# Kernel optimization log

Hardware: AMD Instinct MI355X
Metric: run time of the kernel (lower is better)

## Reference

```python
import jax, jax.numpy as jnp
import numpy as np

B, S, D, H = 2, 2048, 1024, 16
HD = D // H
EPS = 1e-5


def setup_inputs() -> dict:
    key = jax.random.key(0)
    ks = jax.random.split(key, 12)
    n = lambda k, shp, s=0.02: jax.random.normal(k, shp, dtype=jnp.float32) * s
    return {
        "x": jax.random.normal(ks[0], (B, S, D), dtype=jnp.float32),
        "Wq": n(ks[1], (D, D)), "bq": jnp.zeros((D,), jnp.float32),
        "Wk": n(ks[2], (D, D)), "bk": jnp.zeros((D,), jnp.float32),
        "Wv": n(ks[3], (D, D)), "bv": jnp.zeros((D,), jnp.float32),
        "Wo": n(ks[4], (D, D)), "bo": jnp.zeros((D,), jnp.float32),
        "rel_bias": n(ks[5], (H, S, S)),  # relative_position_bias param (window==S)
        "gamma": jnp.ones((D,), jnp.float32),
        "beta": jnp.zeros((D,), jnp.float32),
    }


def reference(x, Wq, bq, Wk, bk, Wv, bv, Wo, bo, rel_bias, gamma, beta):
    b, s, d = x.shape
    # projections (torch Linear: x @ W.T + b), split heads -> (b, h, s, hd)
    def proj(W, bias):
        return (x @ W.T + bias).reshape(b, s, H, HD).transpose(0, 2, 1, 3)
    Q, K, V = proj(Wq, bq), proj(Wk, bk), proj(Wv, bv)

    scores = jnp.einsum("bhqd,bhkd->bhqk", Q, K) / jnp.sqrt(jnp.float32(HD))
    # additive causal mask (-inf strictly above diagonal) + relative position bias
    i = jnp.arange(s)
    causal = jnp.where(i[:, None] >= i[None, :], 0.0, -jnp.inf).astype(scores.dtype)
    scores = scores + causal[None, None] + rel_bias[None, :, :s, :s]

    attn = jax.nn.softmax(scores, axis=-1)  # dropout is identity in eval mode
    attended = jnp.einsum("bhqk,bhkd->bhqd", attn, V)
    attended = attended.transpose(0, 2, 1, 3).reshape(b, s, d)

    out = attended @ Wo.T + bo
    # residual + LayerNorm(eps=1e-5)
    y = out + x
    mu = jnp.mean(y, axis=-1, keepdims=True)
    var = jnp.var(y, axis=-1, keepdims=True)
    return (y - mu) / jnp.sqrt(var + EPS) * gamma + beta
```

## Files before the change

kernel.cpp:

```cpp
#include <hip/hip_runtime.h>

typedef __attribute__((ext_vector_type(8))) short short8;
typedef __attribute__((ext_vector_type(4))) float f32x4;
typedef unsigned short u16;
typedef __attribute__((ext_vector_type(4))) unsigned short u16x4;

#define S_LEN 2048
#define DMODEL 1024
#define NH 16
#define HD 64

static __device__ __forceinline__ u16 f2bf(float f) {
    union { float f; unsigned u; } x; x.f = f;
    unsigned r = x.u + 0x7fffu + ((x.u >> 16) & 1u);
    return (u16)(r >> 16);
}

#define GLD_LDS16(g, l) __builtin_amdgcn_global_load_lds( \
    (const __attribute__((address_space(1))) void*)(g),   \
    (__attribute__((address_space(3))) void*)(l), 16, 0, 0)

#define MFMA16(a, b, c) __builtin_amdgcn_mfma_f32_16x16x32_bf16(a, b, c, 0, 0, 0)

#define LOAD_FENCE() asm volatile("" ::: "memory")

#define TILE_SYNC() do {                                          \
    asm volatile("s_waitcnt vmcnt(4)" ::: "memory");              \
    __builtin_amdgcn_s_barrier();                                 \
    __builtin_amdgcn_sched_barrier(0);                            \
} while (0)

__global__ __launch_bounds__(256) void cast_kernel(const float* __restrict__ in,
                                                   u16* __restrict__ out, int n4) {
    int i = blockIdx.x * 256 + threadIdx.x;
    if (i < n4) {
        const float4 v = reinterpret_cast<const float4*>(in)[i];
        u16x4 o;
        o.x = f2bf(v.x); o.y = f2bf(v.y); o.z = f2bf(v.z); o.w = f2bf(v.w);
        reinterpret_cast<u16x4*>(out)[i] = o;
    }
}

__global__ __launch_bounds__(256) void gemm_qkv_kernel(
    const u16* __restrict__ xbf,
    const u16* __restrict__ wqbf, const u16* __restrict__ wkbf, const u16* __restrict__ wvbf,
    const float* __restrict__ bq, const float* __restrict__ bk, const float* __restrict__ bv,
    u16* __restrict__ qout, u16* __restrict__ kout, u16* __restrict__ vtout)
{
    __shared__ u16 As[128][64];
    __shared__ u16 Bs[128][64];

    const int z = blockIdx.z;
    const u16* __restrict__ W = (z == 0) ? wqbf : (z == 1) ? wkbf : wvbf;
    const float* __restrict__ bias = (z == 0) ? bq : (z == 1) ? bk : bv;

    const int tid  = threadIdx.x;
    const int lane = tid & 63;
    const int wid  = tid >> 6;
    const int wm = (wid >> 1) * 64;
    const int wn = (wid & 1) * 64;
    const int lr = lane & 15;
    const int lg = lane >> 4;

    const int m0 = blockIdx.y * 128;
    const int n0 = blockIdx.x * 128;

    f32x4 acc[4][4] = {};

    for (int kt = 0; kt < DMODEL; kt += 64) {
#pragma unroll
        for (int i = 0; i < 4; ++i) {
            const int c = i * 256 + tid;
            const int row = c >> 3;
            const int kk = (c & 7) * 8;
            GLD_LDS16(xbf + (size_t)(m0 + row) * DMODEL + kt + kk, &As[0][0] + c * 8);
        }
#pragma unroll
        for (int i = 0; i < 4; ++i) {
            const int c = i * 256 + tid;
            const int row = c >> 3;
            const int kk = (c & 7) * 8;
            GLD_LDS16(W + (size_t)(n0 + row) * DMODEL + kt + kk, &Bs[0][0] + c * 8);
        }
        __syncthreads();
#pragma unroll
        for (int ks = 0; ks < 2; ++ks) {
            short8 af[4], bfr[4];
#pragma unroll
            for (int t = 0; t < 4; ++t)
                af[t] = *(const short8*)&As[wm + t * 16 + lr][ks * 32 + lg * 8];
#pragma unroll
            for (int t = 0; t < 4; ++t)
                bfr[t] = *(const short8*)&Bs[wn + t * 16 + lr][ks * 32 + lg * 8];
#pragma unroll
            for (int mt = 0; mt < 4; ++mt)
#pragma unroll
                for (int nt = 0; nt < 4; ++nt)
                    acc[mt][nt] = MFMA16(af[mt], bfr[nt], acc[mt][nt]);
        }
        __syncthreads();
    }

#pragma unroll
    for (int mt = 0; mt < 4; ++mt) {
#pragma unroll
        for (int nt = 0; nt < 4; ++nt) {
            const int n = n0 + wn + nt * 16 + lr;
            const int h = (n >> 6) & (NH - 1);
            const int hd = n & (HD - 1);
            const float bia = bias[n];
#pragma unroll
            for (int r = 0; r < 4; ++r) {
                const int m = m0 + wm + mt * 16 + lg * 4 + r;
                const int bb = m >> 11;
                const int ss = m & (S_LEN - 1);
                const float v = acc[mt][nt][r] + bia;
                const int bh = bb * NH + h;
                if (z == 0) {
                    qout[((size_t)bh * S_LEN + ss) * HD + hd] = f2bf(v * 0.125f);
                } else if (z == 1) {
                    kout[((size_t)bh * S_LEN + ss) * HD + hd] = f2bf(v);
                } else {
                    vtout[((size_t)bh * HD + hd) * S_LEN + ss] = f2bf(v);
                }
            }
        }
    }
}

__global__ __launch_bounds__(256, 3) void attn_kernel(
    const u16* __restrict__ qbf, const u16* __restrict__ kbf,
    const u16* __restrict__ vtbf, const float* __restrict__ rel,
    u16* __restrict__ att)
{
    __shared__ u16 Klds[2][64][64];
    __shared__ u16 Vlds[2][64][64];
    __shared__ u16 P[4][16][72];

    const int tid  = threadIdx.x;
    const int lane = tid & 63;
    const int wid  = tid >> 6;
    const int c = lane & 15;
    const int g = lane >> 4;

    const int h = blockIdx.x >> 1;
    const int b = blockIdx.x & 1;
    const int bh = b * NH + h;
    const int blkq = gridDim.y - 1 - blockIdx.y;
    const int q0 = blkq * 64;
    const int qv = q0 + wid * 16 + c;

    const size_t base = (size_t)bh * S_LEN * HD;

    const short8 qf0 = *(const short8*)&qbf[base + (size_t)qv * HD + g * 8];
    const short8 qf1 = *(const short8*)&qbf[base + (size_t)qv * HD + 32 + g * 8];

    const float* __restrict__ relrow = rel + (size_t)h * S_LEN * S_LEN + (size_t)qv * S_LEN;

    f32x4 o[4] = {};
    float m_run = -3e38f, l_run = 0.f;
    f32x4 rbA[4], rbB[4];

    const int nkt = blkq + 1;

    auto stage = [&](int kt, int bb) {
        const int k0 = kt * 64;
#pragma unroll
        for (int i = 0; i < 2; ++i) {
            const int s = i * 256 + tid;
            const int row = s >> 3;
            const int u = (s & 7) ^ (row & 7);
            GLD_LDS16(kbf + base + (size_t)(k0 + row) * HD + u * 8,
                      &Klds[bb][0][0] + s * 8);
        }
#pragma unroll
        for (int i = 0; i < 2; ++i) {
            const int s = i * 256 + tid;
            const int row = s >> 3;
            const int u = (s & 7) ^ (row & 7);
            GLD_LDS16(vtbf + base + (size_t)row * S_LEN + k0 + u * 8,
                      &Vlds[bb][0][0] + s * 8);
        }
    };

    auto rel_into = [&](f32x4 (&rb)[4], int kt) {
        const float* rn = relrow + kt * 64;
        rb[0] = *(const f32x4*)&rn[g * 4];
        rb[1] = *(const f32x4*)&rn[16 + g * 4];
        rb[2] = *(const f32x4*)&rn[32 + g * 4];
        rb[3] = *(const f32x4*)&rn[48 + g * 4];
    };

    auto compute_tile = [&](int cur, int k0, bool diag, const f32x4 (&rb)[4]) {
        short8 kf[8];
#pragma unroll
        for (int mt = 0; mt < 4; ++mt) {
            const u16* kp = &Klds[cur][0][0] + (mt * 16 + c) * 64;
            kf[2 * mt]     = *(const short8*)(kp + ((g ^ (c & 7)) * 8));
            kf[2 * mt + 1] = *(const short8*)(kp + (((4 + g) ^ (c & 7)) * 8));
        }
        f32x4 st[4] = {};
        __builtin_amdgcn_s_setprio(1);
#pragma unroll
        for (int mt = 0; mt < 4; ++mt) {
            st[mt] = MFMA16(kf[2 * mt], qf0, st[mt]);
            st[mt] = MFMA16(kf[2 * mt + 1], qf1, st[mt]);
        }
        __builtin_amdgcn_s_setprio(0);

        short8 vf[8];
#pragma unroll
        for (int nt = 0; nt < 4; ++nt) {
            const u16* vp = &Vlds[cur][0][0] + (nt * 16 + c) * 64;
            vf[2 * nt]     = *(const short8*)(vp + ((g ^ (c & 7)) * 8));
            vf[2 * nt + 1] = *(const short8*)(vp + (((4 + g) ^ (c & 7)) * 8));
        }

        float tm = -3e38f;
        if (diag) {
#pragma unroll
            for (int mt = 0; mt < 4; ++mt)
#pragma unroll
                for (int r = 0; r < 4; ++r) {
                    const int k = k0 + mt * 16 + g * 4 + r;
                    float sv = st[mt][r] + rb[mt][r];
                    if (k > qv) sv = -1e30f;
                    st[mt][r] = sv;
                    tm = fmaxf(tm, sv);
                }
        } else {
#pragma unroll
            for (int mt = 0; mt < 4; ++mt)
#pragma unroll
                for (int r = 0; r < 4; ++r) {
                    const float sv = st[mt][r] + rb[mt][r];
                    st[mt][r] = sv;
                    tm = fmaxf(tm, sv);
                }
        }
        tm = fmaxf(tm, __shfl_xor(tm, 16));
        tm = fmaxf(tm, __shfl_xor(tm, 32));

        const float mn = fmaxf(m_run, tm);
        const float sc = __expf(m_run - mn);
        m_run = mn;

        float rsum = 0.f;
#pragma unroll
        for (int mt = 0; mt < 4; ++mt)
#pragma unroll
            for (int r = 0; r < 4; ++r) {
                const float e = __expf(st[mt][r] - mn);
                st[mt][r] = e;
                rsum += e;
            }
        rsum += __shfl_xor(rsum, 16);
        rsum += __shfl_xor(rsum, 32);
        l_run = l_run * sc + rsum;

#pragma unroll
        for (int r = 0; r < 4; ++r) {
            const float scq = __shfl(sc, g * 4 + r);
#pragma unroll
            for (int nt = 0; nt < 4; ++nt) o[nt][r] *= scq;
        }

#pragma unroll
        for (int mt = 0; mt < 4; ++mt) {
            u16x4 pk;
            pk.x = f2bf(st[mt][0]);
            pk.y = f2bf(st[mt][1]);
            pk.z = f2bf(st[mt][2]);
            pk.w = f2bf(st[mt][3]);
            *(u16x4*)&P[wid][c][mt * 16 + g * 4] = pk;
        }
        const short8 pa0 = *(const short8*)&P[wid][c][g * 8];
        const short8 pa1 = *(const short8*)&P[wid][c][32 + g * 8];

        __builtin_amdgcn_s_setprio(1);
        o[0] = MFMA16(pa0, vf[0], o[0]);
        o[0] = MFMA16(pa1, vf[1], o[0]);
        o[1] = MFMA16(pa0, vf[2], o[1]);
        o[1] = MFMA16(pa1, vf[3], o[1]);
        o[2] = MFMA16(pa0, vf[4], o[2]);
        o[2] = MFMA16(pa1, vf[5], o[2]);
        o[3] = MFMA16(pa0, vf[6], o[3]);
        o[3] = MFMA16(pa1, vf[7], o[3]);
        __builtin_amdgcn_s_setprio(0);
    };

    stage(0, 0);
    LOAD_FENCE();
    rel_into(rbA, 0);
    __syncthreads();

    int cur = 0;
    int t = 0;
    while (t + 1 < nkt - 1) {
        stage(t + 1, cur ^ 1);
        LOAD_FENCE();
        rel_into(rbB, t + 1);
        LOAD_FENCE();
        compute_tile(cur, t * 64, false, rbA);
        TILE_SYNC();
        cur ^= 1;

        stage(t + 2, cur ^ 1);
        LOAD_FENCE();
        rel_into(rbA, t + 2);
        LOAD_FENCE();
        compute_tile(cur, (t + 1) * 64, false, rbB);
        TILE_SYNC();
        cur ^= 1;

        t += 2;
    }

    if (t < nkt - 1) {
        stage(t + 1, cur ^ 1);
        LOAD_FENCE();
        rel_into(rbB, t + 1);
        LOAD_FENCE();
        compute_tile(cur, t * 64, false, rbA);
        TILE_SYNC();
        cur ^= 1;
        compute_tile(cur, (nkt - 1) * 64, true, rbB);
    } else {
        compute_tile(cur, (nkt - 1) * 64, true, rbA);
    }

#pragma unroll
    for (int r = 0; r < 4; ++r) {
        const float linv = 1.0f / __shfl(l_run, g * 4 + r);
        const int q = q0 + wid * 16 + g * 4 + r;
#pragma unroll
        for (int nt = 0; nt < 4; ++nt) {
            att[((size_t)(b * S_LEN + q)) * DMODEL + h * HD + nt * 16 + c] =
                f2bf(o[nt][r] * linv);
        }
    }
}

__global__ __launch_bounds__(256) void gemm_o_kernel(
    const u16* __restrict__ att, const u16* __restrict__ wobf,
    const float* __restrict__ bo, const float* __restrict__ x,
    float* __restrict__ y)
{
    __shared__ u16 As[128][64];
    __shared__ u16 Bs[128][64];

    const int tid  = threadIdx.x;
    const int lane = tid & 63;
    const int wid  = tid >> 6;
    const int wm = (wid >> 1) * 64;
    const int wn = (wid & 1) * 64;
    const int lr = lane & 15;
    const int lg = lane >> 4;

    const int m0 = blockIdx.y * 128;
    const int n0 = blockIdx.x * 128;

    f32x4 acc[4][4] = {};

    for (int kt = 0; kt < DMODEL; kt += 64) {
#pragma unroll
        for (int i = 0; i < 4; ++i) {
            const int c = i * 256 + tid;
            const int row = c >> 3;
            const int kk = (c & 7) * 8;
            GLD_LDS16(att + (size_t)(m0 + row) * DMODEL + kt + kk, &As[0][0] + c * 8);
        }
#pragma unroll
        for (int i = 0; i < 4; ++i) {
            const int c = i * 256 + tid;
            const int row = c >> 3;
            const int kk = (c & 7) * 8;
            GLD_LDS16(wobf + (size_t)(n0 + row) * DMODEL + kt + kk, &Bs[0][0] + c * 8);
        }
        __syncthreads();
#pragma unroll
        for (int ks = 0; ks < 2; ++ks) {
            short8 af[4], bfr[4];
#pragma unroll
            for (int t = 0; t < 4; ++t)
                af[t] = *(const short8*)&As[wm + t * 16 + lr][ks * 32 + lg * 8];
#pragma unroll
            for (int t = 0; t < 4; ++t)
                bfr[t] = *(const short8*)&Bs[wn + t * 16 + lr][ks * 32 + lg * 8];
#pragma unroll
            for (int mt = 0; mt < 4; ++mt)
#pragma unroll
                for (int nt = 0; nt < 4; ++nt)
                    acc[mt][nt] = MFMA16(af[mt], bfr[nt], acc[mt][nt]);
        }
        __syncthreads();
    }

#pragma unroll
    for (int mt = 0; mt < 4; ++mt) {
#pragma unroll
        for (int nt = 0; nt < 4; ++nt) {
            const int n = n0 + wn + nt * 16 + lr;
            const float bia = bo[n];
#pragma unroll
            for (int r = 0; r < 4; ++r) {
                const int m = m0 + wm + mt * 16 + lg * 4 + r;
                const size_t idx = (size_t)m * DMODEL + n;
                y[idx] = acc[mt][nt][r] + bia + x[idx];
            }
        }
    }
}

__global__ __launch_bounds__(256) void ln_kernel(
    const float* __restrict__ y, const float* __restrict__ gamma,
    const float* __restrict__ beta, float* __restrict__ out)
{
    __shared__ float red[8];
    const int row = blockIdx.x;
    const int tid = threadIdx.x;
    const size_t base = (size_t)row * DMODEL + tid * 4;
    const float4 v = *(const float4*)&y[base];
    float s  = v.x + v.y + v.z + v.w;
    float ss = v.x * v.x + v.y * v.y + v.z * v.z + v.w * v.w;
#pragma unroll
    for (int off = 1; off < 64; off <<= 1) {
        s  += __shfl_xor(s, off);
        ss += __shfl_xor(ss, off);
    }
    const int w = tid >> 6;
    if ((tid & 63) == 0) { red[w] = s; red[4 + w] = ss; }
    __syncthreads();
    s  = red[0] + red[1] + red[2] + red[3];
    ss = red[4] + red[5] + red[6] + red[7];
    const float mu = s * (1.0f / DMODEL);
    const float var = ss * (1.0f / DMODEL) - mu * mu;
    const float rstd = rsqrtf(var + 1e-5f);
    const int col = tid * 4;
    float4 o;
    o.x = (v.x - mu) * rstd * gamma[col + 0] + beta[col + 0];
    o.y = (v.y - mu) * rstd * gamma[col + 1] + beta[col + 1];
    o.z = (v.z - mu) * rstd * gamma[col + 2] + beta[col + 2];
    o.w = (v.w - mu) * rstd * gamma[col + 3] + beta[col + 3];
    *(float4*)&out[base] = o;
}

extern "C" void kernel_launch(void* const* d_in, const int* in_sizes, int n_in,
                              void* d_out, int out_size, void* d_ws, size_t ws_size,
                              hipStream_t stream) {
    (void)in_sizes; (void)n_in; (void)out_size; (void)ws_size;
    const float* x     = (const float*)d_in[0];
    const float* Wq    = (const float*)d_in[1];
    const float* bq    = (const float*)d_in[2];
    const float* Wk    = (const float*)d_in[3];
    const float* bk    = (const float*)d_in[4];
    const float* Wv    = (const float*)d_in[5];
    const float* bv    = (const float*)d_in[6];
    const float* Wo    = (const float*)d_in[7];
    const float* bo    = (const float*)d_in[8];
    const float* rel   = (const float*)d_in[9];
    const float* gamma = (const float*)d_in[10];
    const float* beta  = (const float*)d_in[11];
    float* out = (float*)d_out;

    char* ws = (char*)d_ws;
    u16* xbf   = (u16*)(ws);
    u16* wqbf  = (u16*)(ws + ( 8u << 20));
    u16* wkbf  = (u16*)(ws + (10u << 20));
    u16* wvbf  = (u16*)(ws + (12u << 20));
    u16* wobf  = (u16*)(ws + (14u << 20));
    u16* qbf   = (u16*)(ws + (16u << 20));
    u16* kbf   = (u16*)(ws + (24u << 20));
    u16* vtbf  = (u16*)(ws + (32u << 20));
    u16* attbf = (u16*)(ws + (40u << 20));
    float* y   = (float*)(ws + (48u << 20));

    cast_kernel<<<4096, 256, 0, stream>>>(x,  xbf,  (2 * S_LEN * DMODEL) / 4);
    cast_kernel<<<1024, 256, 0, stream>>>(Wq, wqbf, (DMODEL * DMODEL) / 4);
    cast_kernel<<<1024, 256, 0, stream>>>(Wk, wkbf, (DMODEL * DMODEL) / 4);
    cast_kernel<<<1024, 256, 0, stream>>>(Wv, wvbf, (DMODEL * DMODEL) / 4);
    cast_kernel<<<1024, 256, 0, stream>>>(Wo, wobf, (DMODEL * DMODEL) / 4);

    gemm_qkv_kernel<<<dim3(8, 32, 3), 256, 0, stream>>>(
        xbf, wqbf, wkbf, wvbf, bq, bk, bv, qbf, kbf, vtbf);

    attn_kernel<<<dim3(2 * NH, 32), 256, 0, stream>>>(qbf, kbf, vtbf, rel, attbf);

    gemm_o_kernel<<<dim3(8, 32), 256, 0, stream>>>(attbf, wobf, bo, x, y);

    ln_kernel<<<2 * S_LEN, 256, 0, stream>>>(y, gamma, beta, out);
}
```

Measured before the change: 175.9 us.

## Prefetch relative bias one tile further and merge weight casts into one launch

The attention loop now loads the relative-position bias for tile t+2 after computing tile t, instead of before it. This gives the global loads a full tile of compute to hide behind, and the final iterations use a full vmcnt(0) wait to drain the outstanding loads. Separately, the four weight-cast launches are merged into a single 2D-grid kernel to cut launch overhead. The deeper prefetch keeps more loads in flight, and the wait-count bookkeeping is fragile if the number of outstanding loads per stage does not match vmcnt(4).

```diff
diff --git a/kernel.cpp b/kernel.cpp
--- a/kernel.cpp
+++ b/kernel.cpp
@@ -30,8 +30,31 @@
     __builtin_amdgcn_sched_barrier(0);                            \
 } while (0)
 
+#define TILE_SYNC_FULL() do {                                     \
+    asm volatile("s_waitcnt vmcnt(0)" ::: "memory");              \
+    __builtin_amdgcn_s_barrier();                                 \
+    __builtin_amdgcn_sched_barrier(0);                            \
+} while (0)
+
 __global__ __launch_bounds__(256) void cast_kernel(const float* __restrict__ in,
                                                    u16* __restrict__ out, int n4) {
+    int i = blockIdx.x * 256 + threadIdx.x;
+    if (i < n4) {
+        const float4 v = reinterpret_cast<const float4*>(in)[i];
+        u16x4 o;
+        o.x = f2bf(v.x); o.y = f2bf(v.y); o.z = f2bf(v.z); o.w = f2bf(v.w);
+        reinterpret_cast<u16x4*>(out)[i] = o;
+    }
+}
+
+__global__ __launch_bounds__(256) void cast4_kernel(
+    const float* __restrict__ w0, const float* __restrict__ w1,
+    const float* __restrict__ w2, const float* __restrict__ w3,
+    u16* __restrict__ o0, u16* __restrict__ o1,
+    u16* __restrict__ o2, u16* __restrict__ o3, int n4) {
+    const int z = blockIdx.y;
+    const float* in = (z == 0) ? w0 : (z == 1) ? w1 : (z == 2) ? w2 : w3;
+    u16* out = (z == 0) ? o0 : (z == 1) ? o1 : (z == 2) ? o2 : o3;
     int i = blockIdx.x * 256 + threadIdx.x;
     if (i < n4) {
         const float4 v = reinterpret_cast<const float4*>(in)[i];
@@ -292,6 +315,7 @@
     stage(0, 0);
     LOAD_FENCE();
     rel_into(rbA, 0);
+    if (nkt > 1) rel_into(rbB, 1);
     __syncthreads();
 
     int cur = 0;
@@ -299,18 +323,23 @@
     while (t + 1 < nkt - 1) {
         stage(t + 1, cur ^ 1);
         LOAD_FENCE();
-        rel_into(rbB, t + 1);
+        compute_tile(cur, t * 64, false, rbA);
+        rel_into(rbA, t + 2);
         LOAD_FENCE();
-        compute_tile(cur, t * 64, false, rbA);
         TILE_SYNC();
         cur ^= 1;
 
         stage(t + 2, cur ^ 1);
         LOAD_FENCE();
-        rel_into(rbA, t + 2);
-        LOAD_FENCE();
         compute_tile(cur, (t + 1) * 64, false, rbB);
-        TILE_SYNC();
+        if (t + 3 < nkt) {
+            rel_into(rbB, t + 3);
+            LOAD_FENCE();
+            TILE_SYNC();
+        } else {
+            LOAD_FENCE();
+            TILE_SYNC_FULL();
+        }
         cur ^= 1;
 
         t += 2;
@@ -319,10 +348,8 @@
     if (t < nkt - 1) {
         stage(t + 1, cur ^ 1);
         LOAD_FENCE();
-        rel_into(rbB, t + 1);
-        LOAD_FENCE();
         compute_tile(cur, t * 64, false, rbA);
-        TILE_SYNC();
+        TILE_SYNC_FULL();
         cur ^= 1;
         compute_tile(cur, (nkt - 1) * 64, true, rbB);
     } else {
@@ -475,11 +502,9 @@
     u16* attbf = (u16*)(ws + (40u << 20));
     float* y   = (float*)(ws + (48u << 20));
 
-    cast_kernel<<<4096, 256, 0, stream>>>(x,  xbf,  (2 * S_LEN * DMODEL) / 4);
-    cast_kernel<<<1024, 256, 0, stream>>>(Wq, wqbf, (DMODEL * DMODEL) / 4);
-    cast_kernel<<<1024, 256, 0, stream>>>(Wk, wkbf, (DMODEL * DMODEL) / 4);
-    cast_kernel<<<1024, 256, 0, stream>>>(Wv, wvbf, (DMODEL * DMODEL) / 4);
-    cast_kernel<<<1024, 256, 0, stream>>>(Wo, wobf, (DMODEL * DMODEL) / 4);
+    cast_kernel<<<4096, 256, 0, stream>>>(x, xbf, (2 * S_LEN * DMODEL) / 4);
+    cast4_kernel<<<dim3(1024, 4), 256, 0, stream>>>(
+        Wq, Wk, Wv, Wo, wqbf, wkbf, wvbf, wobf, (DMODEL * DMODEL) / 4);
 
     gemm_qkv_kernel<<<dim3(8, 32, 3), 256, 0, stream>>>(
         xbf, wqbf, wkbf, wvbf, bq, bk, bv, qbf, kbf, vtbf);
```

Measured after the change: 172.6 us. Within noise of the previous version (-1.9%).
